# Kernel tuning notes

Hardware: AMD Instinct MI355X
Metric: run time of the kernel (lower is better)

## Reference

```python
import jax, jax.numpy as jnp
import numpy as np

D_MODEL = 384
D_STATE = 16
D_CONV = 3
EXPAND = 2
D_INNER = EXPAND * D_MODEL          # 768
DT_RANK = (D_MODEL + 15) // 16      # 24 (mamba_ssm 'auto' rank = ceil(d_model/16))
B_, H_, W_ = 8, 32, 32


def setup_inputs() -> dict:
    key = jax.random.key(0)
    ks = jax.random.split(key, 8)
    s = lambda k, shape, scale: jax.random.normal(k, shape, jnp.float32) * scale
    x = jax.random.normal(ks[0], (B_, D_MODEL, H_, W_), jnp.float32)
    in_proj_w = s(ks[1], (2 * D_INNER, D_MODEL), 0.02)
    conv_w = s(ks[2], (D_INNER, D_CONV), 0.1)          # depthwise conv kernels
    conv_b = jnp.zeros((D_INNER,), jnp.float32)
    x_proj_w = s(ks[3], (DT_RANK + 2 * D_STATE, D_INNER), 0.02)
    dt_proj_w = s(ks[4], (D_INNER, DT_RANK), 0.1)
    # bias so that softplus(bias) ~= 0.01 (mamba dt init)
    dt_proj_b = jnp.log(jnp.expm1(jnp.full((D_INNER,), 0.01, jnp.float32)))
    # S4D-real init: A = -[1..N] per channel, stored as log
    A_log = jnp.log(jnp.broadcast_to(
        jnp.arange(1, D_STATE + 1, dtype=jnp.float32), (D_INNER, D_STATE)))
    D = jnp.ones((D_INNER,), jnp.float32)
    out_proj_w = s(ks[5], (D_MODEL, D_INNER), 0.02)
    return dict(x=x, in_proj_w=in_proj_w, conv_w=conv_w, conv_b=conv_b,
                x_proj_w=x_proj_w, dt_proj_w=dt_proj_w, dt_proj_b=dt_proj_b,
                A_log=A_log, D=D, out_proj_w=out_proj_w)


def _mamba(xseq, in_proj_w, conv_w, conv_b, x_proj_w,
           dt_proj_w, dt_proj_b, A_log, D, out_proj_w):
    # xseq: (B, L, d_model)
    B, L, _ = xseq.shape
    xz = xseq @ in_proj_w.T                         # (B, L, 2*d_inner)
    xin, z = jnp.split(xz, 2, axis=-1)

    # depthwise causal conv1d over L
    xc = jnp.transpose(xin, (0, 2, 1))              # (B, d_inner, L)
    xc = jnp.pad(xc, ((0, 0), (0, 0), (D_CONV - 1, 0)))
    xc = jax.lax.conv_general_dilated(
        xc, conv_w[:, None, :], (1,), 'VALID',
        dimension_numbers=('NCH', 'OIH', 'NCH'),
        feature_group_count=D_INNER)
    xc = xc + conv_b[None, :, None]
    u = jax.nn.silu(jnp.transpose(xc, (0, 2, 1)))   # (B, L, d_inner)

    dbc = u @ x_proj_w.T                            # (B, L, dt_rank + 2N)
    dt = dbc[..., :DT_RANK]
    Bm = dbc[..., DT_RANK:DT_RANK + D_STATE]        # (B, L, N)
    Cm = dbc[..., DT_RANK + D_STATE:]               # (B, L, N)
    dt = jax.nn.softplus(dt @ dt_proj_w.T + dt_proj_b)  # (B, L, d_inner)
    A = -jnp.exp(A_log)                             # (d_inner, N)

    def step(h, inp):
        dt_t, B_t, C_t, u_t = inp                   # (B,d), (B,N), (B,N), (B,d)
        dA = jnp.exp(dt_t[..., None] * A)           # (B, d_inner, N)
        h = dA * h + (dt_t * u_t)[..., None] * B_t[:, None, :]
        y = jnp.einsum('bdn,bn->bd', h, C_t)
        return h, y

    h0 = jnp.zeros((B, D_INNER, D_STATE), xseq.dtype)
    _, ys = jax.lax.scan(step, h0, (jnp.swapaxes(dt, 0, 1), jnp.swapaxes(Bm, 0, 1),
                                    jnp.swapaxes(Cm, 0, 1), jnp.swapaxes(u, 0, 1)))
    y = jnp.swapaxes(ys, 0, 1) + u * D              # (B, L, d_inner)
    y = y * jax.nn.silu(z)
    return y @ out_proj_w.T                         # (B, L, d_model)


def reference(x, in_proj_w, conv_w, conv_b, x_proj_w,
              dt_proj_w, dt_proj_b, A_log, D, out_proj_w):
    # x: (B, C, H, W) -> sequence (B, H*W, C) -> Mamba -> back to (B, C, H, W)
    B, C, H, W = x.shape
    xseq = jnp.transpose(x, (0, 2, 3, 1)).reshape(B, H * W, C)
    y = _mamba(xseq, in_proj_w, conv_w, conv_b, x_proj_w,
               dt_proj_w, dt_proj_b, A_log, D, out_proj_w)
    return jnp.transpose(y.reshape(B, H, W, C), (0, 3, 1, 2))
```

## Files before the change

kernel.cpp:

```cpp
#include <hip/hip_runtime.h>

#define D_MODEL 384
#define D_STATE 16
#define D_INNER 768
#define DT_RANK 24
#define NB 8
#define LSEQ 1024
#define NROWS (NB * LSEQ)
#define DBC_N 56
#define SEG 16
#define NSEG 64

typedef unsigned short u16;
typedef __attribute__((ext_vector_type(8))) short bf16x8;
typedef __attribute__((ext_vector_type(4))) float f32x4;

__device__ __forceinline__ float silu(float x) { return x / (1.f + __expf(-x)); }

__device__ __forceinline__ u16 f2bf_rne(float v, float& hval) {
    unsigned u = __builtin_bit_cast(unsigned, v);
    unsigned h = (u + 0x7FFFu + ((u >> 16) & 1u)) >> 16;
    hval = __builtin_bit_cast(float, h << 16);
    return (u16)h;
}

__device__ __forceinline__ void split2(float v, u16& h, u16& l) {
    float hval, dummy;
    h = f2bf_rne(v, hval);
    l = f2bf_rne(v - hval, dummy);
}

template <int CTRL>
__device__ __forceinline__ float dpp_mov(float v) {
    return __builtin_bit_cast(float, __builtin_amdgcn_update_dpp(
        0, __builtin_bit_cast(int, v), CTRL, 0xf, 0xf, false));
}

__global__ __launch_bounds__(256) void k_splitw(const float* __restrict__ src,
                                                u16* __restrict__ hi, u16* __restrict__ lo,
                                                int count) {
    const int i = blockIdx.x * 256 + threadIdx.x;
    if (i >= count) return;
    u16 h, l;
    split2(src[i], h, l);
    hi[i] = h; lo[i] = l;
}

__global__ __launch_bounds__(256) void k_splitw_pad(const float* __restrict__ src,
                                                    u16* __restrict__ hi, u16* __restrict__ lo) {
    const int i = blockIdx.x * 256 + threadIdx.x;
    if (i >= 64 * 768) return;
    const int row = i / 768;
    u16 h = 0, l = 0;
    if (row < DBC_N) split2(src[i], h, l);
    hi[i] = h; lo[i] = l;
}

__global__ __launch_bounds__(256) void k_splitT(const float* __restrict__ src,
                                                u16* __restrict__ hi, u16* __restrict__ lo,
                                                int R) {
    __shared__ float s[32][33];
    const int r0 = blockIdx.x * 32, c0 = blockIdx.y * 32, b = blockIdx.z;
    const int t = threadIdx.x;
    const int cc = t & 31, rr = t >> 5;
#pragma unroll
    for (int p = 0; p < 4; ++p)
        s[rr + p * 8][cc] = src[((size_t)b * R + r0 + rr + p * 8) * LSEQ + c0 + cc];
    __syncthreads();
    const int rr2 = t & 31, cc2 = t >> 5;
#pragma unroll
    for (int p = 0; p < 4; ++p) {
        const int c = cc2 + p * 8;
        u16 h, l;
        split2(s[rr2][c], h, l);
        const size_t idx = ((size_t)b * LSEQ + c0 + c) * R + r0 + rr2;
        hi[idx] = h; lo[idx] = l;
    }
}

template <int K, int MODE>
__global__ __launch_bounds__(256) void k_gemm(const u16* __restrict__ Ahi,
                                              const u16* __restrict__ Alo,
                                              const u16* __restrict__ Bhi,
                                              const u16* __restrict__ Blo,
                                              float* __restrict__ out0,
                                              float* __restrict__ out1) {
    constexpr int KT = K / 32;
    constexpr int NT = 3 * KT;
    __shared__ u16 lA[2][512 * 8];
    __shared__ u16 lB[2][512 * 8];
    const int tid = threadIdx.x;
    const int n0 = blockIdx.x * 128;
    const int m0 = blockIdx.y * 128;

    bf16x8 ra[2], rb[2];
    auto load_tile = [&](int t) {
        const int s = t / KT;
        const int ko = (t - s * KT) * 32;
        const u16* Ab = (s < 2) ? Ahi : Alo;
        const u16* Bb = (s == 1) ? Blo : Bhi;
#pragma unroll
        for (int i = 0; i < 2; ++i) {
            const int slot = tid + 256 * i;
            ra[i] = *reinterpret_cast<const bf16x8*>(
                Ab + (size_t)(m0 + (slot & 127)) * K + ko + (slot >> 7) * 8);
            rb[i] = *reinterpret_cast<const bf16x8*>(
                Bb + (size_t)(n0 + (slot & 127)) * K + ko + (slot >> 7) * 8);
        }
    };
    auto write_tile = [&](int buf) {
#pragma unroll
        for (int i = 0; i < 2; ++i) {
            const int slot = tid + 256 * i;
            *reinterpret_cast<bf16x8*>(&lA[buf][slot * 8]) = ra[i];
            *reinterpret_cast<bf16x8*>(&lB[buf][slot * 8]) = rb[i];
        }
    };

    load_tile(0);
    write_tile(0);
    load_tile(1);

    const int lane = tid & 63, w = tid >> 6;
    const int wm = w >> 1, wn = w & 1;
    const int fr = lane & 15, g = lane >> 4;
    const int abase = (g * 128 + wm * 64 + fr) * 8;
    const int bbase = (g * 128 + wn * 64 + fr) * 8;

    f32x4 acc[4][4] = {};
    for (int t = 0; t < NT; ++t) {
        const int cur = t & 1;
        __syncthreads();
        bf16x8 a[4], b[4];
#pragma unroll
        for (int mi = 0; mi < 4; ++mi)
            a[mi] = *reinterpret_cast<const bf16x8*>(&lA[cur][abase + mi * 128]);
#pragma unroll
        for (int ni = 0; ni < 4; ++ni)
            b[ni] = *reinterpret_cast<const bf16x8*>(&lB[cur][bbase + ni * 128]);
#pragma unroll
        for (int mi = 0; mi < 4; ++mi)
#pragma unroll
            for (int ni = 0; ni < 4; ++ni)
                acc[mi][ni] = __builtin_amdgcn_mfma_f32_16x16x32_bf16(
                    a[mi], b[ni], acc[mi][ni], 0, 0, 0);
        if (t + 1 < NT) {
            __syncthreads();
            write_tile(cur ^ 1);
            if (t + 2 < NT) load_tile(t + 2);
        }
    }

    const int b_idx = m0 >> 10;
    const int l0b = m0 & 1023;
    if (MODE == 0) {
        if (n0 < D_INNER) {
#pragma unroll
            for (int mi = 0; mi < 4; ++mi) {
#pragma unroll
                for (int ni = 0; ni < 4; ++ni) {
                    const int m = m0 + wm * 64 + mi * 16 + (lane >> 4) * 4;
                    const int n = n0 + wn * 64 + ni * 16 + (lane & 15);
#pragma unroll
                    for (int j = 0; j < 4; ++j)
                        out0[(size_t)(m + j) * D_INNER + n] = acc[mi][ni][j];
                }
            }
        } else {
#pragma unroll
            for (int mi = 0; mi < 4; ++mi) {
#pragma unroll
                for (int ni = 0; ni < 4; ++ni) {
                    const int l = l0b + wm * 64 + mi * 16 + (lane >> 4) * 4;
                    const int d = (n0 - D_INNER) + wn * 64 + ni * 16 + (lane & 15);
                    float4 v = make_float4(silu(acc[mi][ni][0]), silu(acc[mi][ni][1]),
                                           silu(acc[mi][ni][2]), silu(acc[mi][ni][3]));
                    *reinterpret_cast<float4*>(
                        &out1[((size_t)b_idx * D_INNER + d) * LSEQ + l]) = v;
                }
            }
        }
    } else {
#pragma unroll
        for (int mi = 0; mi < 4; ++mi) {
#pragma unroll
            for (int ni = 0; ni < 4; ++ni) {
                const int l = l0b + wm * 64 + mi * 16 + (lane >> 4) * 4;
                const int n = n0 + wn * 64 + ni * 16 + (lane & 15);
                float4 v = make_float4(acc[mi][ni][0], acc[mi][ni][1],
                                       acc[mi][ni][2], acc[mi][ni][3]);
                *reinterpret_cast<float4*>(
                    &out0[((size_t)b_idx * D_MODEL + n) * LSEQ + l]) = v;
            }
        }
    }
}

__global__ __launch_bounds__(256) void k_xprojm(const u16* __restrict__ Uhi,
                                                const u16* __restrict__ Ulo,
                                                const u16* __restrict__ Whi,
                                                const u16* __restrict__ Wlo,
                                                float* __restrict__ dbc,
                                                float* __restrict__ bct) {
    __shared__ u16 lA[2][64 * 32];
    __shared__ u16 lB[2][64 * 32];
    const int tid = threadIdx.x;
    const int m0 = blockIdx.x * 64;
    const int arow = tid >> 2, acol = (tid & 3) * 8;

    bf16x8 ra, rb;
    auto load_tile = [&](int t) {
        const int s = t / 24;
        const int ko = (t - s * 24) * 32;
        const u16* Ab = (s < 2) ? Uhi : Ulo;
        const u16* Bb = (s == 1) ? Wlo : Whi;
        ra = *reinterpret_cast<const bf16x8*>(Ab + (size_t)(m0 + arow) * D_INNER + ko + acol);
        rb = *reinterpret_cast<const bf16x8*>(Bb + (size_t)arow * D_INNER + ko + acol);
    };
    auto write_tile = [&](int buf) {
        *reinterpret_cast<bf16x8*>(&lA[buf][arow * 32 + acol]) = ra;
        *reinterpret_cast<bf16x8*>(&lB[buf][arow * 32 + acol]) = rb;
    };

    load_tile(0);
    write_tile(0);
    load_tile(1);

    const int lane = tid & 63, w = tid >> 6;
    const int fr = lane & 15, g = lane >> 4;
    f32x4 acc[4] = {};
    for (int t = 0; t < 72; ++t) {
        const int cur = t & 1;
        __syncthreads();
        bf16x8 a = *reinterpret_cast<const bf16x8*>(&lA[cur][(w * 16 + fr) * 32 + g * 8]);
        bf16x8 b[4];
#pragma unroll
        for (int ni = 0; ni < 4; ++ni)
            b[ni] = *reinterpret_cast<const bf16x8*>(&lB[cur][(ni * 16 + fr) * 32 + g * 8]);
#pragma unroll
        for (int ni = 0; ni < 4; ++ni)
            acc[ni] = __builtin_amdgcn_mfma_f32_16x16x32_bf16(a, b[ni], acc[ni], 0, 0, 0);
        if (t + 1 < 72) {
            __syncthreads();
            write_tile(cur ^ 1);
            if (t + 2 < 72) load_tile(t + 2);
        }
    }

    const int b_idx = m0 >> 10;
#pragma unroll
    for (int ni = 0; ni < 4; ++ni) {
        const int col = ni * 16 + fr;
#pragma unroll
        for (int j = 0; j < 4; ++j) {
            const int r = w * 16 + g * 4 + j;
            const float v = acc[ni][j];
            if (col < DT_RANK) {
                dbc[(size_t)(m0 + r) * DBC_N + col] = v;
            } else if (col < DBC_N) {
                bct[((size_t)b_idx * 32 + (col - DT_RANK)) * LSEQ + ((m0 & 1023) + r)] = v;
            }
        }
    }
}

__global__ __launch_bounds__(256) void k_conv(const float* __restrict__ xin,
                                              const float* __restrict__ cw,
                                              const float* __restrict__ cb,
                                              u16* __restrict__ u_hi,
                                              u16* __restrict__ u_lo,
                                              float* __restrict__ uT) {
    __shared__ float xs[34][32];
    __shared__ float us[32][33];
    const int d0 = blockIdx.x * 32;
    const int l0 = blockIdx.y * 32;
    const int b  = blockIdx.z;
    const int t = threadIdx.x;
    const int dd = t & 31, r = t >> 5;
    for (int rr = r; rr < 34; rr += 8) {
        const int l = l0 - 2 + rr;
        xs[rr][dd] = (l >= 0) ? xin[((size_t)b * LSEQ + l) * D_INNER + d0 + dd] : 0.f;
    }
    __syncthreads();
    const float w0 = cw[(d0 + dd) * 3 + 0], w1 = cw[(d0 + dd) * 3 + 1], w2 = cw[(d0 + dd) * 3 + 2];
    const float bv = cb[d0 + dd];
#pragma unroll
    for (int p = 0; p < 4; ++p) {
        const int li = r + p * 8;
        float acc = bv;
        acc = fmaf(xs[li + 0][dd], w0, acc);
        acc = fmaf(xs[li + 1][dd], w1, acc);
        acc = fmaf(xs[li + 2][dd], w2, acc);
        const float uv = silu(acc);
        u16 h, l;
        split2(uv, h, l);
        const size_t idx = ((size_t)b * LSEQ + l0 + li) * D_INNER + d0 + dd;
        u_hi[idx] = h; u_lo[idx] = l;
        us[li][dd] = uv;
    }
    __syncthreads();
    const int ll = t & 31, dg = t >> 5;
#pragma unroll
    for (int p = 0; p < 4; ++p) {
        const int dl = dg + p * 8;
        uT[((size_t)b * D_INNER + d0 + dl) * LSEQ + l0 + ll] = us[ll][dl];
    }
}

__global__ __launch_bounds__(256) void k_dtproj(const float* __restrict__ dbc,
                                                const float* __restrict__ W,
                                                const float* __restrict__ bias,
                                                float* __restrict__ dtT) {
    __shared__ float sd[64][25];
    __shared__ float sw[64][24];
    __shared__ float sb[64];
    const int d0 = blockIdx.x * 64;
    const int row0 = blockIdx.y * 64;
    const int b = row0 >> 10, lr0 = row0 & 1023;
    const int t = threadIdx.x;
    for (int e = t; e < 64 * 24; e += 256) {
        const int rl = e / 24, rr = e - rl * 24;
        sd[rl][rr] = dbc[(size_t)(row0 + rl) * DBC_N + rr];
        sw[rl][rr] = W[(size_t)(d0 + rl) * DT_RANK + rr];
    }
    if (t < 64) sb[t] = bias[d0 + t];
    __syncthreads();
    const int ll = t & 63, dg = t >> 6;
    for (int dd = 0; dd < 16; ++dd) {
        const int dl = dg * 16 + dd;
        float acc = sb[dl];
#pragma unroll
        for (int r = 0; r < DT_RANK; ++r) acc = fmaf(sd[ll][r], sw[dl][r], acc);
        const float v = (acc > 20.f) ? acc : log1pf(__expf(acc));
        dtT[((size_t)b * D_INNER + d0 + dl) * LSEQ + lr0 + ll] = v;
    }
}

__global__ __launch_bounds__(1024, 8) void k_scan(float* dtyT,
                                                  const float* __restrict__ uT,
                                                  const float* __restrict__ szT,
                                                  const float* __restrict__ bct,
                                                  const float* __restrict__ A_log,
                                                  const float* __restrict__ Dp) {
    __shared__ float dt_s[LSEQ], u_s[LSEQ], sz_s[LSEQ], y_s[LSEQ];
    __shared__ float Pb[16][NSEG + 2], Hb[16][NSEG + 2];
    const int t = threadIdx.x;
    const int d = blockIdx.x;
    const int b = blockIdx.y;
    const size_t base = ((size_t)b * D_INNER + d) * LSEQ;
    if (t < 256) {
        *reinterpret_cast<float4*>(&dt_s[t * 4]) =
            *reinterpret_cast<const float4*>(&dtyT[base + t * 4]);
    } else if (t < 512) {
        const int q = (t - 256) * 4;
        *reinterpret_cast<float4*>(&u_s[q]) = *reinterpret_cast<const float4*>(&uT[base + q]);
    } else if (t < 768) {
        const int q = (t - 512) * 4;
        *reinterpret_cast<float4*>(&sz_s[q]) = *reinterpret_cast<const float4*>(&szT[base + q]);
    }
    const int n = t & 15, seg = t >> 4;
    const float Aval = -__expf(A_log[d * D_STATE + n]);
    const float Dv = Dp[d];
    float Breg[SEG];
    {
        const size_t bb = ((size_t)b * 32 + n) * LSEQ + seg * SEG;
#pragma unroll
        for (int q = 0; q < SEG; q += 4)
            *reinterpret_cast<float4*>(&Breg[q]) = *reinterpret_cast<const float4*>(&bct[bb + q]);
    }
    __syncthreads();
    const int l0 = seg * SEG;
    float h = 0.f, P = 1.f;
#pragma unroll
    for (int l = 0; l < SEG; ++l) {
        const float dtv = dt_s[l0 + l];
        const float a = __expf(dtv * Aval);
        h = fmaf(a, h, dtv * u_s[l0 + l] * Breg[l]);
        P *= a;
    }
    Pb[n][seg] = P;
    Hb[n][seg] = h;
    float Creg[SEG];
    {
        const size_t cc = ((size_t)b * 32 + 16 + n) * LSEQ + seg * SEG;
#pragma unroll
        for (int q = 0; q < SEG; q += 4)
            *reinterpret_cast<float4*>(&Creg[q]) = *reinterpret_cast<const float4*>(&bct[cc + q]);
    }
    __syncthreads();
    {
        const int w = t >> 6, lane = t & 63;
        float Pw = Pb[w][lane], Hw = Hb[w][lane];
#pragma unroll
        for (int off = 1; off < NSEG; off <<= 1) {
            const float Pp = __shfl_up(Pw, off);
            const float Hp = __shfl_up(Hw, off);
            if (lane >= off) {
                Hw = fmaf(Hp, Pw, Hw);
                Pw *= Pp;
            }
        }
        Hb[w][lane] = Hw;
    }
    __syncthreads();
    h = (seg == 0) ? 0.f : Hb[n][seg - 1];
#pragma unroll
    for (int l = 0; l < SEG; ++l) {
        const float dtv = dt_s[l0 + l];
        const float u_v = u_s[l0 + l];
        const float a = __expf(dtv * Aval);
        h = fmaf(a, h, dtv * u_v * Breg[l]);
        float p = h * Creg[l];
        p += dpp_mov<0x128>(p);
        p += dpp_mov<0x124>(p);
        p += dpp_mov<0x122>(p);
        p += dpp_mov<0x121>(p);
        if (n == 0)
            y_s[l0 + l] = fmaf(u_v, Dv, p) * sz_s[l0 + l];
    }
    __syncthreads();
    if (t < 256)
        *reinterpret_cast<float4*>(&dtyT[base + t * 4]) =
            *reinterpret_cast<const float4*>(&y_s[t * 4]);
}

extern "C" void kernel_launch(void* const* d_in, const int* in_sizes, int n_in,
                              void* d_out, int out_size, void* d_ws, size_t ws_size,
                              hipStream_t stream) {
    const float* x         = (const float*)d_in[0];
    const float* in_proj_w = (const float*)d_in[1];
    const float* conv_w    = (const float*)d_in[2];
    const float* conv_b    = (const float*)d_in[3];
    const float* x_proj_w  = (const float*)d_in[4];
    const float* dt_proj_w = (const float*)d_in[5];
    const float* dt_proj_b = (const float*)d_in[6];
    const float* A_log     = (const float*)d_in[7];
    const float* Dp        = (const float*)d_in[8];
    const float* out_proj_w= (const float*)d_in[9];
    float* out = (float*)d_out;

    const size_t SB = (size_t)NROWS * D_INNER * 4;
    char* wsb = (char*)d_ws;
    float* xin   = (float*)(wsb);
    float* szT   = (float*)(wsb + SB);
    u16*  u_hi   = (u16*)  (wsb + 2 * SB);
    u16*  u_lo   = u_hi + (size_t)NROWS * D_INNER;
    float* uT    = (float*)(wsb + 3 * SB);
    float* dbc   = (float*)(wsb + 4 * SB);
    float* bct   = (float*)(wsb + 4 * SB + 1835008);
    u16*  Wi_hi  = (u16*) (wsb + 4 * SB + 1835008 + 1048576);
    u16*  Wi_lo  = Wi_hi + 1536 * 384;
    u16*  Wo_hi  = Wi_lo + 1536 * 384;
    u16*  Wo_lo  = Wo_hi + 384 * 768;
    u16*  Wx_hi  = Wo_lo + 384 * 768;
    u16*  Wx_lo  = Wx_hi + 64 * 768;
    u16*  Ax_hi  = (u16*)uT;
    u16*  Ax_lo  = Ax_hi + (size_t)NROWS * 384;
    u16*  Ay_hi  = (u16*)uT;
    u16*  Ay_lo  = Ay_hi + (size_t)NROWS * 768;
    float* dtyT  = xin;

    k_splitw<<<(1536 * 384 + 255) / 256, 256, 0, stream>>>(in_proj_w, Wi_hi, Wi_lo, 1536 * 384);
    k_splitw<<<(384 * 768 + 255) / 256, 256, 0, stream>>>(out_proj_w, Wo_hi, Wo_lo, 384 * 768);
    k_splitw_pad<<<(64 * 768 + 255) / 256, 256, 0, stream>>>(x_proj_w, Wx_hi, Wx_lo);
    k_splitT<<<dim3(12, 32, NB), 256, 0, stream>>>(x, Ax_hi, Ax_lo, 384);
    k_gemm<384, 0><<<dim3(12, 64), 256, 0, stream>>>(Ax_hi, Ax_lo, Wi_hi, Wi_lo, xin, szT);
    k_conv<<<dim3(24, 32, NB), 256, 0, stream>>>(xin, conv_w, conv_b, u_hi, u_lo, uT);
    k_xprojm<<<NROWS / 64, 256, 0, stream>>>(u_hi, u_lo, Wx_hi, Wx_lo, dbc, bct);
    k_dtproj<<<dim3(12, NROWS / 64), 256, 0, stream>>>(dbc, dt_proj_w, dt_proj_b, dtyT);
    k_scan<<<dim3(D_INNER, NB), 1024, 0, stream>>>(dtyT, uT, szT, bct, A_log, Dp);
    k_splitT<<<dim3(24, 32, NB), 256, 0, stream>>>(dtyT, Ay_hi, Ay_lo, 768);
    k_gemm<768, 1><<<dim3(3, 64), 256, 0, stream>>>(Ay_hi, Ay_lo, Wo_hi, Wo_lo, out, nullptr);
}
```

Baseline: 315.0 us.

## Fuse split-bf16 hi/lo passes into a single K loop in GEMMs

```diff
diff --git a/kernel.cpp b/kernel.cpp
--- a/kernel.cpp
+++ b/kernel.cpp
@@ -86,40 +86,40 @@
                                               float* __restrict__ out0,
                                               float* __restrict__ out1) {
     constexpr int KT = K / 32;
-    constexpr int NT = 3 * KT;
-    __shared__ u16 lA[2][512 * 8];
-    __shared__ u16 lB[2][512 * 8];
+    __shared__ u16 lA[2][2][512 * 8];
+    __shared__ u16 lB[2][2][512 * 8];
     const int tid = threadIdx.x;
     const int n0 = blockIdx.x * 128;
     const int m0 = blockIdx.y * 128;
 
-    bf16x8 ra[2], rb[2];
-    auto load_tile = [&](int t) {
-        const int s = t / KT;
-        const int ko = (t - s * KT) * 32;
-        const u16* Ab = (s < 2) ? Ahi : Alo;
-        const u16* Bb = (s == 1) ? Blo : Bhi;
+    bf16x8 rah[2], ral[2], rbh[2], rbl[2];
+    auto load_kt = [&](int kt) {
+        const int ko = kt * 32;
 #pragma unroll
         for (int i = 0; i < 2; ++i) {
             const int slot = tid + 256 * i;
-            ra[i] = *reinterpret_cast<const bf16x8*>(
-                Ab + (size_t)(m0 + (slot & 127)) * K + ko + (slot >> 7) * 8);
-            rb[i] = *reinterpret_cast<const bf16x8*>(
-                Bb + (size_t)(n0 + (slot & 127)) * K + ko + (slot >> 7) * 8);
+            const size_t aoff = (size_t)(m0 + (slot & 127)) * K + ko + (slot >> 7) * 8;
+            const size_t boff = (size_t)(n0 + (slot & 127)) * K + ko + (slot >> 7) * 8;
+            rah[i] = *reinterpret_cast<const bf16x8*>(Ahi + aoff);
+            ral[i] = *reinterpret_cast<const bf16x8*>(Alo + aoff);
+            rbh[i] = *reinterpret_cast<const bf16x8*>(Bhi + boff);
+            rbl[i] = *reinterpret_cast<const bf16x8*>(Blo + boff);
         }
     };
-    auto write_tile = [&](int buf) {
+    auto write_kt = [&](int buf) {
 #pragma unroll
         for (int i = 0; i < 2; ++i) {
             const int slot = tid + 256 * i;
-            *reinterpret_cast<bf16x8*>(&lA[buf][slot * 8]) = ra[i];
-            *reinterpret_cast<bf16x8*>(&lB[buf][slot * 8]) = rb[i];
+            *reinterpret_cast<bf16x8*>(&lA[buf][0][slot * 8]) = rah[i];
+            *reinterpret_cast<bf16x8*>(&lA[buf][1][slot * 8]) = ral[i];
+            *reinterpret_cast<bf16x8*>(&lB[buf][0][slot * 8]) = rbh[i];
+            *reinterpret_cast<bf16x8*>(&lB[buf][1][slot * 8]) = rbl[i];
         }
     };
 
-    load_tile(0);
-    write_tile(0);
-    load_tile(1);
+    load_kt(0);
+    write_kt(0);
+    if (KT > 1) load_kt(1);
 
     const int lane = tid & 63, w = tid >> 6;
     const int wm = w >> 1, wn = w & 1;
@@ -128,26 +128,35 @@
     const int bbase = (g * 128 + wn * 64 + fr) * 8;
 
     f32x4 acc[4][4] = {};
-    for (int t = 0; t < NT; ++t) {
-        const int cur = t & 1;
+    for (int kt = 0; kt < KT; ++kt) {
+        const int cur = kt & 1;
         __syncthreads();
-        bf16x8 a[4], b[4];
+        bf16x8 ah[4], al[4], bh[4], bl[4];
+#pragma unroll
+        for (int mi = 0; mi < 4; ++mi) {
+            ah[mi] = *reinterpret_cast<const bf16x8*>(&lA[cur][0][abase + mi * 128]);
+            al[mi] = *reinterpret_cast<const bf16x8*>(&lA[cur][1][abase + mi * 128]);
+        }
+#pragma unroll
+        for (int ni = 0; ni < 4; ++ni) {
+            bh[ni] = *reinterpret_cast<const bf16x8*>(&lB[cur][0][bbase + ni * 128]);
+            bl[ni] = *reinterpret_cast<const bf16x8*>(&lB[cur][1][bbase + ni * 128]);
+        }
 #pragma unroll
         for (int mi = 0; mi < 4; ++mi)
-            a[mi] = *reinterpret_cast<const bf16x8*>(&lA[cur][abase + mi * 128]);
-#pragma unroll
-        for (int ni = 0; ni < 4; ++ni)
-            b[ni] = *reinterpret_cast<const bf16x8*>(&lB[cur][bbase + ni * 128]);
-#pragma unroll
-        for (int mi = 0; mi < 4; ++mi)
-#pragma unroll
-            for (int ni = 0; ni < 4; ++ni)
+#pragma unroll
+            for (int ni = 0; ni < 4; ++ni) {
                 acc[mi][ni] = __builtin_amdgcn_mfma_f32_16x16x32_bf16(
-                    a[mi], b[ni], acc[mi][ni], 0, 0, 0);
-        if (t + 1 < NT) {
+                    ah[mi], bh[ni], acc[mi][ni], 0, 0, 0);
+                acc[mi][ni] = __builtin_amdgcn_mfma_f32_16x16x32_bf16(
+                    ah[mi], bl[ni], acc[mi][ni], 0, 0, 0);
+                acc[mi][ni] = __builtin_amdgcn_mfma_f32_16x16x32_bf16(
+                    al[mi], bh[ni], acc[mi][ni], 0, 0, 0);
+            }
+        if (kt + 1 < KT) {
             __syncthreads();
-            write_tile(cur ^ 1);
-            if (t + 2 < NT) load_tile(t + 2);
+            write_kt(cur ^ 1);
+            if (kt + 2 < KT) load_kt(kt + 2);
         }
     }
 
@@ -202,48 +211,59 @@
                                                 const u16* __restrict__ Wlo,
                                                 float* __restrict__ dbc,
                                                 float* __restrict__ bct) {
-    __shared__ u16 lA[2][64 * 32];
-    __shared__ u16 lB[2][64 * 32];
+    __shared__ u16 lA[2][2][64 * 32];
+    __shared__ u16 lB[2][2][64 * 32];
     const int tid = threadIdx.x;
     const int m0 = blockIdx.x * 64;
     const int arow = tid >> 2, acol = (tid & 3) * 8;
 
-    bf16x8 ra, rb;
-    auto load_tile = [&](int t) {
-        const int s = t / 24;
-        const int ko = (t - s * 24) * 32;
-        const u16* Ab = (s < 2) ? Uhi : Ulo;
-        const u16* Bb = (s == 1) ? Wlo : Whi;
-        ra = *reinterpret_cast<const bf16x8*>(Ab + (size_t)(m0 + arow) * D_INNER + ko + acol);
-        rb = *reinterpret_cast<const bf16x8*>(Bb + (size_t)arow * D_INNER + ko + acol);
+    bf16x8 rah, ral, rbh, rbl;
+    auto load_kt = [&](int kt) {
+        const int ko = kt * 32;
+        const size_t aoff = (size_t)(m0 + arow) * D_INNER + ko + acol;
+        const size_t boff = (size_t)arow * D_INNER + ko + acol;
+        rah = *reinterpret_cast<const bf16x8*>(Uhi + aoff);
+        ral = *reinterpret_cast<const bf16x8*>(Ulo + aoff);
+        rbh = *reinterpret_cast<const bf16x8*>(Whi + boff);
+        rbl = *reinterpret_cast<const bf16x8*>(Wlo + boff);
     };
-    auto write_tile = [&](int buf) {
-        *reinterpret_cast<bf16x8*>(&lA[buf][arow * 32 + acol]) = ra;
-        *reinterpret_cast<bf16x8*>(&lB[buf][arow * 32 + acol]) = rb;
+    auto write_kt = [&](int buf) {
+        *reinterpret_cast<bf16x8*>(&lA[buf][0][arow * 32 + acol]) = rah;
+        *reinterpret_cast<bf16x8*>(&lA[buf][1][arow * 32 + acol]) = ral;
+        *reinterpret_cast<bf16x8*>(&lB[buf][0][arow * 32 + acol]) = rbh;
+        *reinterpret_cast<bf16x8*>(&lB[buf][1][arow * 32 + acol]) = rbl;
     };
 
-    load_tile(0);
-    write_tile(0);
-    load_tile(1);
+    load_kt(0);
+    write_kt(0);
+    load_kt(1);
 
     const int lane = tid & 63, w = tid >> 6;
     const int fr = lane & 15, g = lane >> 4;
     f32x4 acc[4] = {};
-    for (int t = 0; t < 72; ++t) {
-        const int cur = t & 1;
+    for (int kt = 0; kt < 24; ++kt) {
+        const int cur = kt & 1;
         __syncthreads();
-        bf16x8 a = *reinterpret_cast<const bf16x8*>(&lA[cur][(w * 16 + fr) * 32 + g * 8]);
-        bf16x8 b[4];
-#pragma unroll
-        for (int ni = 0; ni < 4; ++ni)
-            b[ni] = *reinterpret_cast<const bf16x8*>(&lB[cur][(ni * 16 + fr) * 32 + g * 8]);
-#pragma unroll
-        for (int ni = 0; ni < 4; ++ni)
-            acc[ni] = __builtin_amdgcn_mfma_f32_16x16x32_bf16(a, b[ni], acc[ni], 0, 0, 0);
-        if (t + 1 < 72) {
+        const int af = (w * 16 + fr) * 32 + g * 8;
+        bf16x8 ah = *reinterpret_cast<const bf16x8*>(&lA[cur][0][af]);
+        bf16x8 al = *reinterpret_cast<const bf16x8*>(&lA[cur][1][af]);
+        bf16x8 bh[4], bl[4];
+#pragma unroll
+        for (int ni = 0; ni < 4; ++ni) {
+            const int bf = (ni * 16 + fr) * 32 + g * 8;
+            bh[ni] = *reinterpret_cast<const bf16x8*>(&lB[cur][0][bf]);
+            bl[ni] = *reinterpret_cast<const bf16x8*>(&lB[cur][1][bf]);
+        }
+#pragma unroll
+        for (int ni = 0; ni < 4; ++ni) {
+            acc[ni] = __builtin_amdgcn_mfma_f32_16x16x32_bf16(ah, bh[ni], acc[ni], 0, 0, 0);
+            acc[ni] = __builtin_amdgcn_mfma_f32_16x16x32_bf16(ah, bl[ni], acc[ni], 0, 0, 0);
+            acc[ni] = __builtin_amdgcn_mfma_f32_16x16x32_bf16(al, bh[ni], acc[ni], 0, 0, 0);
+        }
+        if (kt + 1 < 24) {
             __syncthreads();
-            write_tile(cur ^ 1);
-            if (t + 2 < 72) load_tile(t + 2);
+            write_kt(cur ^ 1);
+            if (kt + 2 < 24) load_kt(kt + 2);
         }
     }
 
```

Measured after the change: 288.1 us. 1.09x faster.
